# Kernel tuning notes

Hardware: AMD Instinct MI355X
Metric: run time of the kernel (lower is better)

## Reference

```python
import jax, jax.numpy as jnp
import numpy as np

N, E, G = 50000, 800000, 128
IN, HID, OUT, H = 128, 64, 32, 4
EPS = 1e-5


def _bn(x, g, b, m, v):
    # BatchNorm1d in eval mode: normalize with running stats
    return (x - m) * jax.lax.rsqrt(v + EPS) * g + b


def _gat(x, src, dst, W, att_src, att_dst, bias, n):
    # PyG GATConv, concat=False: mean over heads
    h = (x @ W).reshape(n, H, -1)                      # [N,H,C]
    a_src = (h * att_src).sum(-1)                      # [N,H]
    a_dst = (h * att_dst).sum(-1)                      # [N,H]
    e = jax.nn.leaky_relu(a_src[src] + a_dst[dst], 0.2)  # [E,H]
    m = jax.ops.segment_max(e, dst, num_segments=n)    # segment softmax over incoming edges
    e = jnp.exp(e - m[dst])
    s = jax.ops.segment_sum(e, dst, num_segments=n)
    alpha = e / s[dst]                                  # [E,H]
    out = jax.ops.segment_sum(alpha[:, :, None] * h[src], dst, num_segments=n)  # [N,H,C]
    return out.mean(axis=1) + bias


def setup_inputs() -> dict:
    key = jax.random.key(0)
    ks = jax.random.split(key, 20)
    d = {
        "x": jax.random.normal(ks[0], (N, IN), jnp.float32),
        "edge_index": jax.random.randint(ks[1], (2, E), 0, N),
        "batch": jnp.sort(jax.random.randint(ks[2], (N,), 0, G)),
        # input_norm
        "in_gamma": jax.random.normal(ks[3], (IN,)) * 0.05 + 1.0,
        "in_beta": jax.random.normal(ks[4], (IN,)) * 0.05,
        "in_mean": jax.random.normal(ks[5], (IN,)) * 0.05,
        "in_var": jax.random.uniform(ks[6], (IN,)) + 0.5,
        # gat1
        "W1": jax.random.normal(ks[7], (IN, H * HID)) * (1.0 / np.sqrt(IN)),
        "as1": jax.random.normal(ks[8], (H, HID)) * 0.1,
        "ad1": jax.random.normal(ks[9], (H, HID)) * 0.1,
        "b1": jnp.zeros((HID,)),
        "bn1_g": jnp.ones((HID,)),
        "bn1_b": jnp.zeros((HID,)),
        "bn1_m": jax.random.normal(ks[10], (HID,)) * 0.05,
        "bn1_v": jax.random.uniform(ks[11], (HID,)) + 0.5,
        # gat2
        "W2": jax.random.normal(ks[12], (HID, H * HID)) * (1.0 / np.sqrt(HID)),
        "as2": jax.random.normal(ks[13], (H, HID)) * 0.1,
        "ad2": jax.random.normal(ks[14], (H, HID)) * 0.1,
        "b2": jnp.zeros((HID,)),
        "bn2_g": jnp.ones((HID,)),
        "bn2_b": jnp.zeros((HID,)),
        "bn2_m": jax.random.normal(ks[15], (HID,)) * 0.05,
        "bn2_v": jax.random.uniform(ks[16], (HID,)) + 0.5,
        # head
        "fc1_w": jax.random.normal(ks[17], (HID, HID // 2)) * (1.0 / np.sqrt(HID)),
        "fc1_b": jnp.zeros((HID // 2,)),
        "fc2_w": jax.random.normal(ks[18], (HID // 2, OUT)) * (1.0 / np.sqrt(HID // 2)),
        "fc2_b": jnp.zeros((OUT,)),
    }
    return d


def reference(x, edge_index, batch, in_gamma, in_beta, in_mean, in_var,
              W1, as1, ad1, b1, bn1_g, bn1_b, bn1_m, bn1_v,
              W2, as2, ad2, b2, bn2_g, bn2_b, bn2_m, bn2_v,
              fc1_w, fc1_b, fc2_w, fc2_b):
    n = x.shape[0]
    # PyG GATConv adds self-loops by default
    loop = jnp.arange(n)
    src = jnp.concatenate([edge_index[0], loop])
    dst = jnp.concatenate([edge_index[1], loop])

    h = _bn(x, in_gamma, in_beta, in_mean, in_var)
    h = _gat(h, src, dst, W1, as1, ad1, b1, n)
    h = jax.nn.relu(_bn(h, bn1_g, bn1_b, bn1_m, bn1_v))
    # dropout p=0.3 is identity in eval mode
    h = _gat(h, src, dst, W2, as2, ad2, b2, n)
    h = jax.nn.relu(_bn(h, bn2_g, bn2_b, bn2_m, bn2_v))

    # global mean pool over graphs
    sums = jax.ops.segment_sum(h, batch, num_segments=G)
    cnts = jax.ops.segment_sum(jnp.ones((n,), h.dtype), batch, num_segments=G)
    emb = sums / jnp.maximum(cnts, 1.0)[:, None]

    out = jax.nn.relu(emb @ fc1_w + fc1_b)
    return out @ fc2_w + fc2_b
```

## Files before the change

kernel.cpp:

```cpp
#include <hip/hip_runtime.h>
#include <hip/hip_bf16.h>

#define EPS   1e-5f
#define NH    4
#define DIN   128
#define DHID  64
#define DOUT  32
#define PNODES 256
#define CAP   128
#define GM    32
#define NBUCK 64
#define BSTR  16
#define EPT   16
#define EPB   (256 * EPT)

typedef __attribute__((ext_vector_type(8))) short short8;
typedef __attribute__((ext_vector_type(4))) float f32x4;
typedef __attribute__((ext_vector_type(2))) float f32x2;

__device__ __forceinline__ float us2f(unsigned short u) {
    return __uint_as_float((unsigned)u << 16);
}
__device__ __forceinline__ unsigned short f2us(float v) {
    __hip_bfloat16 hb = __float2bfloat16(v);
    return *(unsigned short*)&hb;
}
__device__ __forceinline__ unsigned char f2e4m3(float v) {
    int p = __builtin_amdgcn_cvt_pk_fp8_f32(v, 0.f, 0, false);
    return (unsigned char)(p & 0xff);
}
__device__ __forceinline__ float lrelu(float a) { return (a >= 0.f) ? a : 0.2f * a; }

__global__ void k_init0(int* __restrict__ deg, float* __restrict__ pool,
                        int* __restrict__ bcur, int N, int npool) {
    int g = blockIdx.x * blockDim.x + threadIdx.x;
    if (g < N) deg[g] = 1;
    if (g < npool) pool[g] = 0.f;
    if (g < NBUCK * BSTR) bcur[g] = 0;
}

__global__ __launch_bounds__(256) void k_scan_a(const int* __restrict__ deg,
                                                int* __restrict__ rowptr,
                                                int* __restrict__ bsum, int N) {
    __shared__ int sh[256];
    const int t = threadIdx.x;
    const int i = blockIdx.x * 256 + t;
    int v = (i < N) ? deg[i] : 0;
    sh[t] = v;
    __syncthreads();
    #pragma unroll
    for (int o = 1; o < 256; o <<= 1) {
        int u = (t >= o) ? sh[t - o] : 0;
        __syncthreads();
        sh[t] += u;
        __syncthreads();
    }
    if (i < N) rowptr[i] = sh[t] - v;
    if (t == 255) bsum[blockIdx.x] = sh[255];
}

__global__ __launch_bounds__(256) void k_scan_b(int* __restrict__ bsum, int nb) {
    __shared__ int sh[256];
    const int t = threadIdx.x;
    int v = (t < nb) ? bsum[t] : 0;
    sh[t] = v;
    __syncthreads();
    #pragma unroll
    for (int o = 1; o < 256; o <<= 1) {
        int u = (t >= o) ? sh[t - o] : 0;
        __syncthreads();
        sh[t] += u;
        __syncthreads();
    }
    if (t < nb) bsum[t] = sh[t] - v;
}

__global__ __launch_bounds__(256) void k_scan_c(int* __restrict__ rowptr,
                                                int* __restrict__ cursor,
                                                const int* __restrict__ bsum,
                                                int N, int Etot) {
    const int i = blockIdx.x * 256 + threadIdx.x;
    if (i < N) {
        int v = rowptr[i] + bsum[blockIdx.x];
        rowptr[i] = v;
        cursor[i] = v;
    }
    if (i == 0) rowptr[N] = Etot;
}

__global__ __launch_bounds__(256) void k_part(
    const int* __restrict__ ei, int E, int N, int bshift,
    unsigned long long* __restrict__ arena, int* __restrict__ bcur,
    int* __restrict__ deg, int cap)
{
    __shared__ int lhist[NBUCK];
    __shared__ int lbase[NBUCK];
    const int t = threadIdx.x;
    const int e0 = blockIdx.x * EPB;
    const int eEnd = min(e0 + EPB, E + N);

    if (t < NBUCK) lhist[t] = 0;
    __syncthreads();

    int myb[EPT], myd[EPT], mys[EPT];
    #pragma unroll
    for (int r = 0; r < EPT; ++r) {
        int e = e0 + r * 256 + t;
        myb[r] = -1;
        if (e < eEnd) {
            int s, d;
            if (e < E) { s = ei[e]; d = ei[E + e]; atomicAdd(&deg[d], 1); }
            else       { s = d = e - E; }
            int b = d >> bshift;
            myb[r] = b; myd[r] = d; mys[r] = s;
            atomicAdd(&lhist[b], 1);
        }
    }
    __syncthreads();

    if (t < NBUCK) {
        int c = lhist[t];
        lbase[t] = c ? atomicAdd(&bcur[t * BSTR], c) : 0;
        lhist[t] = 0;
    }
    __syncthreads();

    #pragma unroll
    for (int r = 0; r < EPT; ++r) {
        int b = myb[r];
        if (b >= 0) {
            int li = atomicAdd(&lhist[b], 1);
            int pos = lbase[b] + li;
            if (pos >= cap) pos = cap - 1;
            arena[(size_t)b * cap + pos] =
                ((unsigned long long)(unsigned)myd[r] << 32) | (unsigned)mys[r];
        }
    }
}

__global__ __launch_bounds__(256) void k_fill2(
    const unsigned long long* __restrict__ arena, const int* __restrict__ bcur,
    int cap, int* __restrict__ cursor, int* __restrict__ col)
{
    const int b = blockIdx.x;
    const int idx = blockIdx.y * 256 + threadIdx.x;
    if (idx >= bcur[b * BSTR]) return;
    unsigned long long v = arena[(size_t)b * cap + idx];
    int d = (int)(v >> 32);
    int s = (int)(v & 0xffffffffu);
    int pos = atomicAdd(&cursor[d], 1);
    col[pos] = s;
}

__global__ __launch_bounds__(256) void k_prep(
    const float* __restrict__ x,
    const float* __restrict__ ing, const float* __restrict__ inb,
    const float* __restrict__ inm, const float* __restrict__ inv,
    const float* __restrict__ W1, const float* __restrict__ W2,
    const float* __restrict__ as1, const float* __restrict__ ad1,
    const float* __restrict__ as2, const float* __restrict__ ad2,
    const float* __restrict__ b1,
    const float* __restrict__ bn1g, const float* __restrict__ bn1b,
    const float* __restrict__ bn1m, const float* __restrict__ bn1v,
    unsigned short* __restrict__ A, unsigned short* __restrict__ Wt,
    unsigned short* __restrict__ Wt2,
    unsigned short* __restrict__ Wast1, unsigned short* __restrict__ Wast2,
    float* __restrict__ scl1, float* __restrict__ shf1, int N)
{
    int g = blockIdx.x * blockDim.x + threadIdx.x;
    int totA = N * (DIN / 4);
    if (g < totA) {
        int n = g >> 5, k4 = (g & 31) * 4;
        float4 xv = *(const float4*)(x + (size_t)n * DIN + k4);
        float4 gm = *(const float4*)(ing + k4);
        float4 bb = *(const float4*)(inb + k4);
        float4 mm = *(const float4*)(inm + k4);
        float4 vv = *(const float4*)(inv + k4);
        ushort4 o;
        o.x = f2us((xv.x - mm.x) * rsqrtf(vv.x + EPS) * gm.x + bb.x);
        o.y = f2us((xv.y - mm.y) * rsqrtf(vv.y + EPS) * gm.y + bb.y);
        o.z = f2us((xv.z - mm.z) * rsqrtf(vv.z + EPS) * gm.z + bb.z);
        o.w = f2us((xv.w - mm.w) * rsqrtf(vv.w + EPS) * gm.w + bb.w);
        *(ushort4*)(A + (size_t)n * DIN + k4) = o;
    }
    if (g < 256 * DIN) {
        int n = g >> 7, k = g & 127;
        Wt[g] = f2us(W1[(size_t)k * 256 + n]);
    }
    if (g < 256 * DHID) {
        int n = g >> 6, k = g & 63;
        Wt2[g] = f2us(W2[(size_t)k * 256 + n]);
    }
    if (g < 16 * DIN) {
        int c = g >> 7, k = g & 127;
        float s = 0.f;
        if (c < 4)      { for (int j = 0; j < 64; ++j) s += W1[(size_t)k * 256 + c * 64 + j] * as1[c * 64 + j]; }
        else if (c < 8) { for (int j = 0; j < 64; ++j) s += W1[(size_t)k * 256 + (c - 4) * 64 + j] * ad1[(c - 4) * 64 + j]; }
        Wast1[g] = f2us(s);
    }
    if (g < 16 * DHID) {
        int c = g >> 6, k = g & 63;
        float s = 0.f;
        if (c < 4)      { for (int j = 0; j < 64; ++j) s += W2[(size_t)k * 256 + c * 64 + j] * as2[c * 64 + j]; }
        else if (c < 8) { for (int j = 0; j < 64; ++j) s += W2[(size_t)k * 256 + (c - 4) * 64 + j] * ad2[(c - 4) * 64 + j]; }
        Wast2[g] = f2us(s);
    }
    if (g < DHID) {
        float sc = bn1g[g] * rsqrtf(bn1v[g] + EPS);
        scl1[g] = sc;
        shf1[g] = (b1[g] - bn1m[g]) * sc + bn1b[g];
    }
}

__global__ __launch_bounds__(256) void k_gemm1(
    const unsigned short* __restrict__ A,
    const unsigned short* __restrict__ Wt,
    const unsigned short* __restrict__ Wast,
    unsigned char* __restrict__ h,
    float* __restrict__ asrc, float* __restrict__ adst, int N)
{
    __shared__ float Csh[GM][260];
    const int t = threadIdx.x;
    const int lane = t & 63, wv = t >> 6;
    const int qm = lane & 15, qd = lane >> 4;
    const int base = blockIdx.x * GM;

    short8 afr[2][4];
    #pragma unroll
    for (int rt = 0; rt < 2; ++rt) {
        int node = base + rt * 16 + qm;
        if (node >= N) node = N - 1;
        const unsigned short* ap = A + (size_t)node * DIN + qd * 8;
        #pragma unroll
        for (int ks = 0; ks < 4; ++ks)
            afr[rt][ks] = *(const short8*)(ap + ks * 32);
    }

    const int n0 = wv * 64;
    f32x4 acc[2][4];
    #pragma unroll
    for (int rt = 0; rt < 2; ++rt)
        #pragma unroll
        for (int ct = 0; ct < 4; ++ct)
            acc[rt][ct] = (f32x4){0.f, 0.f, 0.f, 0.f};

    #pragma unroll
    for (int ct = 0; ct < 4; ++ct) {
        const unsigned short* bp = Wt + (size_t)(n0 + ct * 16 + qm) * DIN + qd * 8;
        #pragma unroll
        for (int ks = 0; ks < 4; ++ks) {
            short8 bfr = *(const short8*)(bp + ks * 32);
            acc[0][ct] = __builtin_amdgcn_mfma_f32_16x16x32_bf16(afr[0][ks], bfr, acc[0][ct], 0, 0, 0);
            acc[1][ct] = __builtin_amdgcn_mfma_f32_16x16x32_bf16(afr[1][ks], bfr, acc[1][ct], 0, 0, 0);
        }
    }

    {
        const unsigned short* wp = Wast + (size_t)qm * DIN + qd * 8;
        f32x4 aat[2];
        aat[0] = (f32x4){0.f, 0.f, 0.f, 0.f};
        aat[1] = (f32x4){0.f, 0.f, 0.f, 0.f};
        #pragma unroll
        for (int ks = 0; ks < 4; ++ks) {
            short8 wfr = *(const short8*)(wp + ks * 32);
            aat[0] = __builtin_amdgcn_mfma_f32_16x16x32_bf16(afr[0][ks], wfr, aat[0], 0, 0, 0);
            aat[1] = __builtin_amdgcn_mfma_f32_16x16x32_bf16(afr[1][ks], wfr, aat[1], 0, 0, 0);
        }
        const int c = qm;
        #pragma unroll
        for (int rt = 0; rt < 2; ++rt)
            #pragma unroll
            for (int rg = 0; rg < 4; ++rg) {
                int nd = base + rt * 16 + qd * 4 + rg;
                if (nd < N) {
                    if (c < 4)      asrc[nd * 4 + c] = aat[rt][rg];
                    else if (c < 8) adst[nd * 4 + (c - 4)] = aat[rt][rg];
                }
            }
    }

    #pragma unroll
    for (int rt = 0; rt < 2; ++rt)
        #pragma unroll
        for (int ct = 0; ct < 4; ++ct)
            #pragma unroll
            for (int rg = 0; rg < 4; ++rg)
                Csh[rt * 16 + qd * 4 + rg][n0 + ct * 16 + qm] = acc[rt][ct][rg];
    __syncthreads();

    const int hcol = ((t & 3) << 6) | (t >> 2);
    for (int r = 0; r < GM; ++r) {
        int node = base + r;
        if (node >= N) break;
        h[(size_t)node * 256 + t] = f2e4m3(Csh[r][hcol]);
    }
}

__global__ __launch_bounds__(256) void k_gemm2(
    const unsigned short* __restrict__ A2,
    const unsigned short* __restrict__ Wt2,
    const unsigned short* __restrict__ Wast,
    unsigned char* __restrict__ h,
    float* __restrict__ asrc, float* __restrict__ adst, int N)
{
    __shared__ float Csh[GM][260];
    const int t = threadIdx.x;
    const int lane = t & 63, wv = t >> 6;
    const int qm = lane & 15, qd = lane >> 4;
    const int base = blockIdx.x * GM;

    short8 afr[2][2];
    #pragma unroll
    for (int rt = 0; rt < 2; ++rt) {
        int node = base + rt * 16 + qm;
        if (node >= N) node = N - 1;
        const unsigned short* ap = A2 + (size_t)node * DHID + qd * 8;
        #pragma unroll
        for (int ks = 0; ks < 2; ++ks)
            afr[rt][ks] = *(const short8*)(ap + ks * 32);
    }

    const int n0 = wv * 64;
    f32x4 acc[2][4];
    #pragma unroll
    for (int rt = 0; rt < 2; ++rt)
        #pragma unroll
        for (int ct = 0; ct < 4; ++ct)
            acc[rt][ct] = (f32x4){0.f, 0.f, 0.f, 0.f};

    #pragma unroll
    for (int ct = 0; ct < 4; ++ct) {
        const unsigned short* bp = Wt2 + (size_t)(n0 + ct * 16 + qm) * DHID + qd * 8;
        #pragma unroll
        for (int ks = 0; ks < 2; ++ks) {
            short8 bfr = *(const short8*)(bp + ks * 32);
            acc[0][ct] = __builtin_amdgcn_mfma_f32_16x16x32_bf16(afr[0][ks], bfr, acc[0][ct], 0, 0, 0);
            acc[1][ct] = __builtin_amdgcn_mfma_f32_16x16x32_bf16(afr[1][ks], bfr, acc[1][ct], 0, 0, 0);
        }
    }

    {
        const unsigned short* wp = Wast + (size_t)qm * DHID + qd * 8;
        f32x4 aat[2];
        aat[0] = (f32x4){0.f, 0.f, 0.f, 0.f};
        aat[1] = (f32x4){0.f, 0.f, 0.f, 0.f};
        #pragma unroll
        for (int ks = 0; ks < 2; ++ks) {
            short8 wfr = *(const short8*)(wp + ks * 32);
            aat[0] = __builtin_amdgcn_mfma_f32_16x16x32_bf16(afr[0][ks], wfr, aat[0], 0, 0, 0);
            aat[1] = __builtin_amdgcn_mfma_f32_16x16x32_bf16(afr[1][ks], wfr, aat[1], 0, 0, 0);
        }
        const int c = qm;
        #pragma unroll
        for (int rt = 0; rt < 2; ++rt)
            #pragma unroll
            for (int rg = 0; rg < 4; ++rg) {
                int nd = base + rt * 16 + qd * 4 + rg;
                if (nd < N) {
                    if (c < 4)      asrc[nd * 4 + c] = aat[rt][rg];
                    else if (c < 8) adst[nd * 4 + (c - 4)] = aat[rt][rg];
                }
            }
    }

    #pragma unroll
    for (int rt = 0; rt < 2; ++rt)
        #pragma unroll
        for (int ct = 0; ct < 4; ++ct)
            #pragma unroll
            for (int rg = 0; rg < 4; ++rg)
                Csh[rt * 16 + qd * 4 + rg][n0 + ct * 16 + qm] = acc[rt][ct][rg];
    __syncthreads();

    const int hcol = ((t & 3) << 6) | (t >> 2);
    for (int r = 0; r < GM; ++r) {
        int node = base + r;
        if (node >= N) break;
        h[(size_t)node * 256 + t] = f2e4m3(Csh[r][hcol]);
    }
}

__global__ __launch_bounds__(256) void k_agg(
    const int* __restrict__ rowptr, const int* __restrict__ col,
    const float* __restrict__ asrc, const float* __restrict__ adst,
    const unsigned char* __restrict__ h8,
    float* __restrict__ outf, unsigned short* __restrict__ outb,
    const float* __restrict__ scl, const float* __restrict__ shf,
    int mode, int N)
{
    __shared__ float4 exs[4][CAP];
    __shared__ int    cols[4][CAP];
    const int lane = threadIdx.x & 63;
    const int wv   = threadIdx.x >> 6;
    const int d = (blockIdx.x << 2) + wv;
    if (d >= N) return;
    const int r0  = rowptr[d];
    const int deg = rowptr[d + 1] - r0;

    const float4 ad4 = ((const float4*)adst)[d];
    const float4* __restrict__ as4 = (const float4*)asrc;

    float sm0 = 0.f, sm1 = 0.f, sm2 = 0.f, sm3 = 0.f;
    for (int j = lane; j < deg; j += 64) {
        int s = col[r0 + j];
        float4 a = as4[s];
        float e0 = __expf(lrelu(a.x + ad4.x));
        float e1 = __expf(lrelu(a.y + ad4.y));
        float e2 = __expf(lrelu(a.z + ad4.z));
        float e3 = __expf(lrelu(a.w + ad4.w));
        if (j < CAP) { cols[wv][j] = s; exs[wv][j] = make_float4(e0, e1, e2, e3); }
        sm0 += e0; sm1 += e1; sm2 += e2; sm3 += e3;
    }
    #pragma unroll
    for (int o = 1; o < 64; o <<= 1) {
        sm0 += __shfl_xor(sm0, o, 64);
        sm1 += __shfl_xor(sm1, o, 64);
        sm2 += __shfl_xor(sm2, o, 64);
        sm3 += __shfl_xor(sm3, o, 64);
    }
    const float i0 = 0.25f / sm0, i1 = 0.25f / sm1, i2 = 0.25f / sm2, i3 = 0.25f / sm3;

    const unsigned int* __restrict__ hu = (const unsigned int*)h8;
    float a0 = 0.f, a1 = 0.f, a2 = 0.f, a3 = 0.f;
    float b0 = 0.f, b1 = 0.f, b2 = 0.f, b3 = 0.f;
    if (deg <= CAP) {
        int j = 0;
        for (; j + 3 < deg; j += 4) {
            int sA = cols[wv][j],     sB = cols[wv][j + 1];
            int sC = cols[wv][j + 2], sD = cols[wv][j + 3];
            unsigned int vA = hu[(size_t)sA * 64 + lane];
            unsigned int vB = hu[(size_t)sB * 64 + lane];
            unsigned int vC = hu[(size_t)sC * 64 + lane];
            unsigned int vD = hu[(size_t)sD * 64 + lane];
            float4 wA = exs[wv][j],     wB = exs[wv][j + 1];
            float4 wC = exs[wv][j + 2], wD = exs[wv][j + 3];
            f32x2 lA = __builtin_amdgcn_cvt_pk_f32_fp8(vA, false), hA = __builtin_amdgcn_cvt_pk_f32_fp8(vA, true);
            f32x2 lB = __builtin_amdgcn_cvt_pk_f32_fp8(vB, false), hB = __builtin_amdgcn_cvt_pk_f32_fp8(vB, true);
            f32x2 lC = __builtin_amdgcn_cvt_pk_f32_fp8(vC, false), hC = __builtin_amdgcn_cvt_pk_f32_fp8(vC, true);
            f32x2 lD = __builtin_amdgcn_cvt_pk_f32_fp8(vD, false), hD = __builtin_amdgcn_cvt_pk_f32_fp8(vD, true);
            a0 += wA.x * lA.x; a1 += wA.y * lA.y; a2 += wA.z * hA.x; a3 += wA.w * hA.y;
            b0 += wB.x * lB.x; b1 += wB.y * lB.y; b2 += wB.z * hB.x; b3 += wB.w * hB.y;
            a0 += wC.x * lC.x; a1 += wC.y * lC.y; a2 += wC.z * hC.x; a3 += wC.w * hC.y;
            b0 += wD.x * lD.x; b1 += wD.y * lD.y; b2 += wD.z * hD.x; b3 += wD.w * hD.y;
        }
        for (; j < deg; ++j) {
            int s = cols[wv][j];
            unsigned int v = hu[(size_t)s * 64 + lane];
            float4 w = exs[wv][j];
            f32x2 lo = __builtin_amdgcn_cvt_pk_f32_fp8(v, false), hi = __builtin_amdgcn_cvt_pk_f32_fp8(v, true);
            a0 += w.x * lo.x; a1 += w.y * lo.y; a2 += w.z * hi.x; a3 += w.w * hi.y;
        }
    } else {
        for (int j = 0; j < deg; ++j) {
            int s; float4 w;
            if (j < CAP) { s = cols[wv][j]; w = exs[wv][j]; }
            else {
                s = col[r0 + j];
                float4 a = as4[s];
                w.x = __expf(lrelu(a.x + ad4.x)); w.y = __expf(lrelu(a.y + ad4.y));
                w.z = __expf(lrelu(a.z + ad4.z)); w.w = __expf(lrelu(a.w + ad4.w));
            }
            unsigned int v = hu[(size_t)s * 64 + lane];
            f32x2 lo = __builtin_amdgcn_cvt_pk_f32_fp8(v, false), hi = __builtin_amdgcn_cvt_pk_f32_fp8(v, true);
            a0 += w.x * lo.x; a1 += w.y * lo.y; a2 += w.z * hi.x; a3 += w.w * hi.y;
        }
    }
    float acc = (a0 + b0) * i0 + (a1 + b1) * i1 + (a2 + b2) * i2 + (a3 + b3) * i3;

    if (mode) {
        float v = fmaxf(acc * scl[lane] + shf[lane], 0.f);
        outb[(size_t)d * 64 + lane] = f2us(v);
    } else {
        outf[(size_t)d * 64 + lane] = acc;
    }
}

__global__ __launch_bounds__(256) void k_pool(
    const float* __restrict__ outacc,
    const float* __restrict__ b2_,
    const float* __restrict__ bg, const float* __restrict__ bb,
    const float* __restrict__ bm, const float* __restrict__ bv,
    const int* __restrict__ batch,
    float* __restrict__ pool, float* __restrict__ cnt, int N)
{
    const int lane = threadIdx.x & 63;
    const int wave = threadIdx.x >> 6;
    const int base = blockIdx.x * PNODES;
    int end = base + PNODES; if (end > N) end = N;

    const float scale = bg[lane] * rsqrtf(bv[lane] + EPS);
    const float shift = (b2_[lane] - bm[lane]) * scale + bb[lane];

    float acc = 0.f;
    int cur = -1, cl = 0;
    for (int n = base + wave; n < end; n += 4) {
        int gr = batch[n];
        if (gr != cur) {
            if (cur >= 0) {
                atomicAdd(&pool[cur * 64 + lane], acc);
                if (lane == 0) atomicAdd(&cnt[cur], (float)cl);
            }
            cur = gr; acc = 0.f; cl = 0;
        }
        float v = fmaxf(outacc[(size_t)n * 64 + lane] * scale + shift, 0.f);
        acc += v; ++cl;
    }
    if (cur >= 0) {
        atomicAdd(&pool[cur * 64 + lane], acc);
        if (lane == 0) atomicAdd(&cnt[cur], (float)cl);
    }
}

__global__ void k_head(const float* __restrict__ pool, const float* __restrict__ cnt,
                       const float* __restrict__ fc1w, const float* __restrict__ fc1b,
                       const float* __restrict__ fc2w, const float* __restrict__ fc2b,
                       float* __restrict__ out)
{
    int g = blockIdx.x;
    int t = threadIdx.x;
    __shared__ float emb[64];
    __shared__ float z1[32];
    float c = fmaxf(cnt[g], 1.0f);
    emb[t] = pool[g * 64 + t] / c;
    __syncthreads();
    if (t < 32) {
        float s = fc1b[t];
        for (int k = 0; k < 64; ++k) s += emb[k] * fc1w[k * 32 + t];
        z1[t] = fmaxf(s, 0.f);
    }
    __syncthreads();
    if (t < 32) {
        float o = fc2b[t];
        for (int j = 0; j < 32; ++j) o += z1[j] * fc2w[j * 32 + t];
        out[g * 32 + t] = o;
    }
}

extern "C" void kernel_launch(void* const* d_in, const int* in_sizes, int n_in,
                              void* d_out, int out_size, void* d_ws, size_t ws_size,
                              hipStream_t stream)
{
    const float* x    = (const float*)d_in[0];
    const int*   ei   = (const int*)d_in[1];
    const int*   batch= (const int*)d_in[2];
    const float* ing  = (const float*)d_in[3];
    const float* inb  = (const float*)d_in[4];
    const float* inm  = (const float*)d_in[5];
    const float* inv  = (const float*)d_in[6];
    const float* W1   = (const float*)d_in[7];
    const float* as1  = (const float*)d_in[8];
    const float* ad1  = (const float*)d_in[9];
    const float* b1   = (const float*)d_in[10];
    const float* bn1g = (const float*)d_in[11];
    const float* bn1b = (const float*)d_in[12];
    const float* bn1m = (const float*)d_in[13];
    const float* bn1v = (const float*)d_in[14];
    const float* W2   = (const float*)d_in[15];
    const float* as2  = (const float*)d_in[16];
    const float* ad2  = (const float*)d_in[17];
    const float* b2   = (const float*)d_in[18];
    const float* bn2g = (const float*)d_in[19];
    const float* bn2b = (const float*)d_in[20];
    const float* bn2m = (const float*)d_in[21];
    const float* bn2v = (const float*)d_in[22];
    const float* fc1w = (const float*)d_in[23];
    const float* fc1b = (const float*)d_in[24];
    const float* fc2w = (const float*)d_in[25];
    const float* fc2b = (const float*)d_in[26];

    const int N = in_sizes[0] / DIN;
    const int E = in_sizes[1] / 2;
    const int G = out_size / DOUT;
    const int Etot = E + N;

    int bshift = 0;
    while ((N >> bshift) >= NBUCK) ++bshift;
    const int cap = (int)(((long long)Etot << bshift) / N * 5 / 4) + 512;

    unsigned char* h8 = (unsigned char*)d_ws;
    float* asrc   = (float*)(h8 + (size_t)N * 256);
    float* adst   = asrc + (size_t)N * NH;
    unsigned short* Wt    = (unsigned short*)(adst + (size_t)N * NH);
    unsigned short* Wt2   = Wt + 256 * DIN;
    unsigned short* Wast1 = Wt2 + 256 * DHID;
    unsigned short* Wast2 = Wast1 + 16 * DIN;
    float* scl1   = (float*)(Wast2 + 16 * DHID);
    float* shf1   = scl1 + DHID;
    float* outacc = shf1 + DHID;
    unsigned short* A  = (unsigned short*)outacc;
    unsigned short* A2 = (unsigned short*)outacc;
    int*   deg    = (int*)(outacc + (size_t)N * DHID);
    int*   rowptr = deg + N;
    int*   cursor = rowptr + N + 1;
    int*   col    = cursor + N;
    float* pool   = (float*)(col + Etot);
    float* cnt    = pool + (size_t)G * DHID;
    int*   bsum   = (int*)(cnt + G);
    int*   bcur   = (int*)(((size_t)(bsum + 256) + 63) & ~(size_t)63);
    unsigned long long* arena =
        (unsigned long long*)(((size_t)(bcur + NBUCK * BSTR) + 7) & ~(size_t)7);

    const int npool = G * DHID + G;
    const int nScanBlk = (N + 255) / 256;
    dim3 b256(256);

    k_init0<<<(N + 255) / 256, b256, 0, stream>>>(deg, pool, bcur, N, npool);
    k_part<<<(Etot + EPB - 1) / EPB, b256, 0, stream>>>(ei, E, N, bshift, arena, bcur, deg, cap);
    k_scan_a<<<nScanBlk, b256, 0, stream>>>(deg, rowptr, bsum, N);
    k_scan_b<<<1, b256, 0, stream>>>(bsum, nScanBlk);
    k_scan_c<<<nScanBlk, b256, 0, stream>>>(rowptr, cursor, bsum, N, Etot);
    {
        dim3 gFill(NBUCK, (cap + 255) / 256);
        k_fill2<<<gFill, b256, 0, stream>>>(arena, bcur, cap, cursor, col);
    }

    const int prepThreads = N * (DIN / 4);
    k_prep<<<(prepThreads + 255) / 256, b256, 0, stream>>>(
        x, ing, inb, inm, inv, W1, W2, as1, ad1, as2, ad2,
        b1, bn1g, bn1b, bn1m, bn1v,
        A, Wt, Wt2, Wast1, Wast2, scl1, shf1, N);

    k_gemm1<<<(N + GM - 1) / GM, b256, 0, stream>>>(A, Wt, Wast1, h8, asrc, adst, N);
    k_agg<<<(N + 3) / 4, b256, 0, stream>>>(rowptr, col, asrc, adst, h8,
                                            (float*)nullptr, A2, scl1, shf1, 1, N);

    k_gemm2<<<(N + GM - 1) / GM, b256, 0, stream>>>(A2, Wt2, Wast2, h8, asrc, adst, N);
    k_agg<<<(N + 3) / 4, b256, 0, stream>>>(rowptr, col, asrc, adst, h8,
                                            outacc, (unsigned short*)nullptr,
                                            (const float*)nullptr, (const float*)nullptr, 0, N);

    k_pool<<<(N + PNODES - 1) / PNODES, b256, 0, stream>>>(outacc, b2, bn2g, bn2b, bn2m, bn2v,
                                                           batch, pool, cnt, N);
    k_head<<<G, 64, 0, stream>>>(pool, cnt, fc1w, fc1b, fc2w, fc2b, (float*)d_out);
}
```

Before: 360.1 us.

## Fuse CSR build and prep into one persistent kernel; fold input BN into GEMM1

The separate init, partition, three scan, fill and prep kernels are merged into one persistent 256-block kernel that uses software grid barriers between phases. The input BatchNorm is precomputed as per-feature scale and shift and applied inside GEMM1 while loading x, so the bf16 normalized copy of x is no longer written and re-read. This removes several kernel launches and a full pass over the activations. In exchange, the phases run on a fixed grid of 256 blocks, and the spin barriers assume all blocks are resident at once; the fill phase also walks the buckets one after another.

```diff
diff --git a/kernel.cpp b/kernel.cpp
--- a/kernel.cpp
+++ b/kernel.cpp
@@ -13,6 +13,7 @@
 #define BSTR  16
 #define EPT   16
 #define EPB   (256 * EPT)
+#define NBLD  256
 
 typedef __attribute__((ext_vector_type(8))) short short8;
 typedef __attribute__((ext_vector_type(4))) float f32x4;
@@ -31,129 +32,25 @@
 }
 __device__ __forceinline__ float lrelu(float a) { return (a >= 0.f) ? a : 0.2f * a; }
 
-__global__ void k_init0(int* __restrict__ deg, float* __restrict__ pool,
-                        int* __restrict__ bcur, int N, int npool) {
-    int g = blockIdx.x * blockDim.x + threadIdx.x;
-    if (g < N) deg[g] = 1;
-    if (g < npool) pool[g] = 0.f;
-    if (g < NBUCK * BSTR) bcur[g] = 0;
-}
-
-__global__ __launch_bounds__(256) void k_scan_a(const int* __restrict__ deg,
-                                                int* __restrict__ rowptr,
-                                                int* __restrict__ bsum, int N) {
-    __shared__ int sh[256];
-    const int t = threadIdx.x;
-    const int i = blockIdx.x * 256 + t;
-    int v = (i < N) ? deg[i] : 0;
-    sh[t] = v;
+__device__ __forceinline__ void gbar(int* bar, int nblk) {
     __syncthreads();
-    #pragma unroll
-    for (int o = 1; o < 256; o <<= 1) {
-        int u = (t >= o) ? sh[t - o] : 0;
-        __syncthreads();
-        sh[t] += u;
-        __syncthreads();
-    }
-    if (i < N) rowptr[i] = sh[t] - v;
-    if (t == 255) bsum[blockIdx.x] = sh[255];
-}
-
-__global__ __launch_bounds__(256) void k_scan_b(int* __restrict__ bsum, int nb) {
-    __shared__ int sh[256];
-    const int t = threadIdx.x;
-    int v = (t < nb) ? bsum[t] : 0;
-    sh[t] = v;
+    if (threadIdx.x == 0) {
+        __threadfence();
+        int arrive = __hip_atomic_fetch_add(bar, 1, __ATOMIC_RELAXED, __HIP_MEMORY_SCOPE_AGENT);
+        int target = (arrive / nblk + 1) * nblk;
+        while (__hip_atomic_load(bar, __ATOMIC_RELAXED, __HIP_MEMORY_SCOPE_AGENT) < target)
+            __builtin_amdgcn_s_sleep(2);
+        __threadfence();
+    }
     __syncthreads();
-    #pragma unroll
-    for (int o = 1; o < 256; o <<= 1) {
-        int u = (t >= o) ? sh[t - o] : 0;
-        __syncthreads();
-        sh[t] += u;
-        __syncthreads();
-    }
-    if (t < nb) bsum[t] = sh[t] - v;
-}
-
-__global__ __launch_bounds__(256) void k_scan_c(int* __restrict__ rowptr,
-                                                int* __restrict__ cursor,
-                                                const int* __restrict__ bsum,
-                                                int N, int Etot) {
-    const int i = blockIdx.x * 256 + threadIdx.x;
-    if (i < N) {
-        int v = rowptr[i] + bsum[blockIdx.x];
-        rowptr[i] = v;
-        cursor[i] = v;
-    }
-    if (i == 0) rowptr[N] = Etot;
-}
-
-__global__ __launch_bounds__(256) void k_part(
-    const int* __restrict__ ei, int E, int N, int bshift,
+}
+
+__global__ __launch_bounds__(256) void k_build(
+    const int* __restrict__ ei, int E, int N, int bshift, int cap,
     unsigned long long* __restrict__ arena, int* __restrict__ bcur,
-    int* __restrict__ deg, int cap)
-{
-    __shared__ int lhist[NBUCK];
-    __shared__ int lbase[NBUCK];
-    const int t = threadIdx.x;
-    const int e0 = blockIdx.x * EPB;
-    const int eEnd = min(e0 + EPB, E + N);
-
-    if (t < NBUCK) lhist[t] = 0;
-    __syncthreads();
-
-    int myb[EPT], myd[EPT], mys[EPT];
-    #pragma unroll
-    for (int r = 0; r < EPT; ++r) {
-        int e = e0 + r * 256 + t;
-        myb[r] = -1;
-        if (e < eEnd) {
-            int s, d;
-            if (e < E) { s = ei[e]; d = ei[E + e]; atomicAdd(&deg[d], 1); }
-            else       { s = d = e - E; }
-            int b = d >> bshift;
-            myb[r] = b; myd[r] = d; mys[r] = s;
-            atomicAdd(&lhist[b], 1);
-        }
-    }
-    __syncthreads();
-
-    if (t < NBUCK) {
-        int c = lhist[t];
-        lbase[t] = c ? atomicAdd(&bcur[t * BSTR], c) : 0;
-        lhist[t] = 0;
-    }
-    __syncthreads();
-
-    #pragma unroll
-    for (int r = 0; r < EPT; ++r) {
-        int b = myb[r];
-        if (b >= 0) {
-            int li = atomicAdd(&lhist[b], 1);
-            int pos = lbase[b] + li;
-            if (pos >= cap) pos = cap - 1;
-            arena[(size_t)b * cap + pos] =
-                ((unsigned long long)(unsigned)myd[r] << 32) | (unsigned)mys[r];
-        }
-    }
-}
-
-__global__ __launch_bounds__(256) void k_fill2(
-    const unsigned long long* __restrict__ arena, const int* __restrict__ bcur,
-    int cap, int* __restrict__ cursor, int* __restrict__ col)
-{
-    const int b = blockIdx.x;
-    const int idx = blockIdx.y * 256 + threadIdx.x;
-    if (idx >= bcur[b * BSTR]) return;
-    unsigned long long v = arena[(size_t)b * cap + idx];
-    int d = (int)(v >> 32);
-    int s = (int)(v & 0xffffffffu);
-    int pos = atomicAdd(&cursor[d], 1);
-    col[pos] = s;
-}
-
-__global__ __launch_bounds__(256) void k_prep(
-    const float* __restrict__ x,
+    int* __restrict__ deg, int* __restrict__ rowptr, int* __restrict__ cursor,
+    int* __restrict__ col, int* __restrict__ bsum, int* __restrict__ bar,
+    float* __restrict__ pool, int npool,
     const float* __restrict__ ing, const float* __restrict__ inb,
     const float* __restrict__ inm, const float* __restrict__ inv,
     const float* __restrict__ W1, const float* __restrict__ W2,
@@ -162,58 +59,156 @@
     const float* __restrict__ b1,
     const float* __restrict__ bn1g, const float* __restrict__ bn1b,
     const float* __restrict__ bn1m, const float* __restrict__ bn1v,
-    unsigned short* __restrict__ A, unsigned short* __restrict__ Wt,
-    unsigned short* __restrict__ Wt2,
+    unsigned short* __restrict__ Wt, unsigned short* __restrict__ Wt2,
     unsigned short* __restrict__ Wast1, unsigned short* __restrict__ Wast2,
-    float* __restrict__ scl1, float* __restrict__ shf1, int N)
+    float* __restrict__ scl1, float* __restrict__ shf1,
+    float* __restrict__ sclX, float* __restrict__ shfX)
 {
-    int g = blockIdx.x * blockDim.x + threadIdx.x;
-    int totA = N * (DIN / 4);
-    if (g < totA) {
-        int n = g >> 5, k4 = (g & 31) * 4;
-        float4 xv = *(const float4*)(x + (size_t)n * DIN + k4);
-        float4 gm = *(const float4*)(ing + k4);
-        float4 bb = *(const float4*)(inb + k4);
-        float4 mm = *(const float4*)(inm + k4);
-        float4 vv = *(const float4*)(inv + k4);
-        ushort4 o;
-        o.x = f2us((xv.x - mm.x) * rsqrtf(vv.x + EPS) * gm.x + bb.x);
-        o.y = f2us((xv.y - mm.y) * rsqrtf(vv.y + EPS) * gm.y + bb.y);
-        o.z = f2us((xv.z - mm.z) * rsqrtf(vv.z + EPS) * gm.z + bb.z);
-        o.w = f2us((xv.w - mm.w) * rsqrtf(vv.w + EPS) * gm.w + bb.w);
-        *(ushort4*)(A + (size_t)n * DIN + k4) = o;
-    }
-    if (g < 256 * DIN) {
-        int n = g >> 7, k = g & 127;
-        Wt[g] = f2us(W1[(size_t)k * 256 + n]);
-    }
-    if (g < 256 * DHID) {
-        int n = g >> 6, k = g & 63;
-        Wt2[g] = f2us(W2[(size_t)k * 256 + n]);
-    }
-    if (g < 16 * DIN) {
+    __shared__ int sh[256];
+    __shared__ int lhist[NBUCK];
+    __shared__ int lbase[NBUCK];
+    const int t   = threadIdx.x;
+    const int gid = blockIdx.x * 256 + t;
+    const int gsz = gridDim.x * 256;
+    const int nblk = gridDim.x;
+    const int Etot = E + N;
+
+    for (int g = gid; g < N; g += gsz) deg[g] = 1;
+    for (int g = gid; g < npool; g += gsz) pool[g] = 0.f;
+    for (int g = gid; g < NBUCK * BSTR; g += gsz) bcur[g] = 0;
+    for (int g = gid; g < 256 * DIN; g += gsz)
+        Wt[g] = f2us(W1[(size_t)(g & 127) * 256 + (g >> 7)]);
+    for (int g = gid; g < 256 * DHID; g += gsz)
+        Wt2[g] = f2us(W2[(size_t)(g & 63) * 256 + (g >> 6)]);
+    for (int g = gid; g < 16 * DIN; g += gsz) {
         int c = g >> 7, k = g & 127;
         float s = 0.f;
         if (c < 4)      { for (int j = 0; j < 64; ++j) s += W1[(size_t)k * 256 + c * 64 + j] * as1[c * 64 + j]; }
         else if (c < 8) { for (int j = 0; j < 64; ++j) s += W1[(size_t)k * 256 + (c - 4) * 64 + j] * ad1[(c - 4) * 64 + j]; }
         Wast1[g] = f2us(s);
     }
-    if (g < 16 * DHID) {
+    for (int g = gid; g < 16 * DHID; g += gsz) {
         int c = g >> 6, k = g & 63;
         float s = 0.f;
         if (c < 4)      { for (int j = 0; j < 64; ++j) s += W2[(size_t)k * 256 + c * 64 + j] * as2[c * 64 + j]; }
         else if (c < 8) { for (int j = 0; j < 64; ++j) s += W2[(size_t)k * 256 + (c - 4) * 64 + j] * ad2[(c - 4) * 64 + j]; }
         Wast2[g] = f2us(s);
     }
-    if (g < DHID) {
+    for (int g = gid; g < DHID; g += gsz) {
         float sc = bn1g[g] * rsqrtf(bn1v[g] + EPS);
         scl1[g] = sc;
         shf1[g] = (b1[g] - bn1m[g]) * sc + bn1b[g];
     }
+    for (int g = gid; g < DIN; g += gsz) {
+        float sc = ing[g] * rsqrtf(inv[g] + EPS);
+        sclX[g] = sc;
+        shfX[g] = inb[g] - inm[g] * sc;
+    }
+
+    gbar(bar, nblk);
+
+    const int nchP = (Etot + EPB - 1) / EPB;
+    for (int ch = blockIdx.x; ch < nchP; ch += nblk) {
+        const int e0 = ch * EPB;
+        const int eEnd = min(e0 + EPB, Etot);
+        if (t < NBUCK) lhist[t] = 0;
+        __syncthreads();
+        int myb[EPT], myd[EPT], mys[EPT];
+        #pragma unroll
+        for (int r = 0; r < EPT; ++r) {
+            int e = e0 + r * 256 + t;
+            myb[r] = -1;
+            if (e < eEnd) {
+                int s, d;
+                if (e < E) { s = ei[e]; d = ei[E + e]; atomicAdd(&deg[d], 1); }
+                else       { s = d = e - E; }
+                myb[r] = d >> bshift; myd[r] = d; mys[r] = s;
+                atomicAdd(&lhist[myb[r]], 1);
+            }
+        }
+        __syncthreads();
+        if (t < NBUCK) {
+            int c = lhist[t];
+            lbase[t] = c ? atomicAdd(&bcur[t * BSTR], c) : 0;
+            lhist[t] = 0;
+        }
+        __syncthreads();
+        #pragma unroll
+        for (int r = 0; r < EPT; ++r) {
+            int b = myb[r];
+            if (b >= 0) {
+                int li = atomicAdd(&lhist[b], 1);
+                int pos = lbase[b] + li;
+                if (pos >= cap) pos = cap - 1;
+                arena[(size_t)b * cap + pos] =
+                    ((unsigned long long)(unsigned)myd[r] << 32) | (unsigned)mys[r];
+            }
+        }
+        __syncthreads();
+    }
+
+    gbar(bar, nblk);
+
+    const int nchS = (N + 255) / 256;
+    for (int cb = blockIdx.x; cb < nchS; cb += nblk) {
+        int i = cb * 256 + t;
+        int v = (i < N) ? deg[i] : 0;
+        sh[t] = v;
+        __syncthreads();
+        #pragma unroll
+        for (int o = 1; o < 256; o <<= 1) {
+            int u = (t >= o) ? sh[t - o] : 0;
+            __syncthreads();
+            sh[t] += u;
+            __syncthreads();
+        }
+        if (i < N) rowptr[i] = sh[t] - v;
+        if (t == 255) bsum[cb] = sh[255];
+        __syncthreads();
+    }
+
+    gbar(bar, nblk);
+
+    if (blockIdx.x == 0) {
+        int v = (t < nchS) ? bsum[t] : 0;
+        sh[t] = v;
+        __syncthreads();
+        #pragma unroll
+        for (int o = 1; o < 256; o <<= 1) {
+            int u = (t >= o) ? sh[t - o] : 0;
+            __syncthreads();
+            sh[t] += u;
+            __syncthreads();
+        }
+        if (t < nchS) bsum[t] = sh[t] - v;
+    }
+
+    gbar(bar, nblk);
+
+    for (int i = gid; i < N; i += gsz) {
+        int v = rowptr[i] + bsum[i >> 8];
+        rowptr[i] = v;
+        cursor[i] = v;
+    }
+    if (gid == 0) rowptr[N] = Etot;
+
+    gbar(bar, nblk);
+
+    for (int b = 0; b < NBUCK; ++b) {
+        const int cnt = bcur[b * BSTR];
+        const unsigned long long* ap = arena + (size_t)b * cap;
+        for (int idx = gid; idx < cnt; idx += gsz) {
+            unsigned long long v = ap[idx];
+            int d = (int)(v >> 32);
+            int pos = atomicAdd(&cursor[d], 1);
+            col[pos] = (int)(v & 0xffffffffu);
+        }
+    }
 }
 
 __global__ __launch_bounds__(256) void k_gemm1(
-    const unsigned short* __restrict__ A,
+    const float* __restrict__ x,
+    const float* __restrict__ sclX, const float* __restrict__ shfX,
     const unsigned short* __restrict__ Wt,
     const unsigned short* __restrict__ Wast,
     unsigned char* __restrict__ h,
@@ -227,13 +222,23 @@
 
     short8 afr[2][4];
     #pragma unroll
-    for (int rt = 0; rt < 2; ++rt) {
-        int node = base + rt * 16 + qm;
-        if (node >= N) node = N - 1;
-        const unsigned short* ap = A + (size_t)node * DIN + qd * 8;
-        #pragma unroll
-        for (int ks = 0; ks < 4; ++ks)
-            afr[rt][ks] = *(const short8*)(ap + ks * 32);
+    for (int ks = 0; ks < 4; ++ks) {
+        const int k0 = qd * 8 + ks * 32;
+        float4 s0 = *(const float4*)(sclX + k0), s1 = *(const float4*)(sclX + k0 + 4);
+        float4 h0 = *(const float4*)(shfX + k0), h1 = *(const float4*)(shfX + k0 + 4);
+        #pragma unroll
+        for (int rt = 0; rt < 2; ++rt) {
+            int node = base + rt * 16 + qm;
+            if (node >= N) node = N - 1;
+            const float* xp = x + (size_t)node * DIN + k0;
+            float4 x0 = *(const float4*)xp, x1 = *(const float4*)(xp + 4);
+            short8 v;
+            v[0] = f2us(x0.x * s0.x + h0.x); v[1] = f2us(x0.y * s0.y + h0.y);
+            v[2] = f2us(x0.z * s0.z + h0.z); v[3] = f2us(x0.w * s0.w + h0.w);
+            v[4] = f2us(x1.x * s1.x + h1.x); v[5] = f2us(x1.y * s1.y + h1.y);
+            v[6] = f2us(x1.z * s1.z + h1.z); v[7] = f2us(x1.w * s1.w + h1.w);
+            afr[rt][ks] = v;
+        }
     }
 
     const int n0 = wv * 64;
@@ -586,8 +591,9 @@
     unsigned short* Wast2 = Wast1 + 16 * DIN;
     float* scl1   = (float*)(Wast2 + 16 * DHID);
     float* shf1   = scl1 + DHID;
-    float* outacc = shf1 + DHID;
-    unsigned short* A  = (unsigned short*)outacc;
+    float* sclX   = shf1 + DHID;
+    float* shfX   = sclX + DIN;
+    float* outacc = shfX + DIN;
     unsigned short* A2 = (unsigned short*)outacc;
     int*   deg    = (int*)(outacc + (size_t)N * DHID);
     int*   rowptr = deg + N;
@@ -596,31 +602,22 @@
     float* pool   = (float*)(col + Etot);
     float* cnt    = pool + (size_t)G * DHID;
     int*   bsum   = (int*)(cnt + G);
-    int*   bcur   = (int*)(((size_t)(bsum + 256) + 63) & ~(size_t)63);
+    int*   bar    = (int*)(((size_t)(bsum + 256) + 63) & ~(size_t)63);
+    int*   bcur   = bar + 16;
     unsigned long long* arena =
         (unsigned long long*)(((size_t)(bcur + NBUCK * BSTR) + 7) & ~(size_t)7);
 
     const int npool = G * DHID + G;
-    const int nScanBlk = (N + 255) / 256;
     dim3 b256(256);
 
-    k_init0<<<(N + 255) / 256, b256, 0, stream>>>(deg, pool, bcur, N, npool);
-    k_part<<<(Etot + EPB - 1) / EPB, b256, 0, stream>>>(ei, E, N, bshift, arena, bcur, deg, cap);
-    k_scan_a<<<nScanBlk, b256, 0, stream>>>(deg, rowptr, bsum, N);
-    k_scan_b<<<1, b256, 0, stream>>>(bsum, nScanBlk);
-    k_scan_c<<<nScanBlk, b256, 0, stream>>>(rowptr, cursor, bsum, N, Etot);
-    {
-        dim3 gFill(NBUCK, (cap + 255) / 256);
-        k_fill2<<<gFill, b256, 0, stream>>>(arena, bcur, cap, cursor, col);
-    }
-
-    const int prepThreads = N * (DIN / 4);
-    k_prep<<<(prepThreads + 255) / 256, b256, 0, stream>>>(
-        x, ing, inb, inm, inv, W1, W2, as1, ad1, as2, ad2,
+    hipMemsetAsync(bar, 0, 4, stream);
+    k_build<<<dim3(NBLD), b256, 0, stream>>>(
+        ei, E, N, bshift, cap, arena, bcur, deg, rowptr, cursor, col, bsum, bar,
+        pool, npool, ing, inb, inm, inv, W1, W2, as1, ad1, as2, ad2,
         b1, bn1g, bn1b, bn1m, bn1v,
-        A, Wt, Wt2, Wast1, Wast2, scl1, shf1, N);
-
-    k_gemm1<<<(N + GM - 1) / GM, b256, 0, stream>>>(A, Wt, Wast1, h8, asrc, adst, N);
+        Wt, Wt2, Wast1, Wast2, scl1, shf1, sclX, shfX);
+
+    k_gemm1<<<(N + GM - 1) / GM, b256, 0, stream>>>(x, sclX, shfX, Wt, Wast1, h8, asrc, adst, N);
     k_agg<<<(N + 3) / 4, b256, 0, stream>>>(rowptr, col, asrc, adst, h8,
                                             (float*)nullptr, A2, scl1, shf1, 1, N);
 
```

Measured after the change: 488.4 us. +35.6%, slower.
